# Kernel tuning notes

Hardware: AMD Instinct MI355X
Metric: run time of the kernel (lower is better)

## Reference

```python
import jax, jax.numpy as jnp
import numpy as np
import math

B, S, D = 1, 2048, 2048
H, HD, KV = 16, 128, 1
E, F, TOPK = 8, 4096, 2
EPS = 1e-5


def setup_inputs() -> dict:
    key = jax.random.key(0)
    ks = jax.random.split(key, 14)
    sc = 0.02
    inp = {
        "x": jax.random.normal(ks[0], (B, S, D), dtype=jnp.float32),
        "wq": jax.random.normal(ks[1], (D, H * HD), dtype=jnp.float32) * sc,
        "wk": jax.random.normal(ks[2], (D, KV * HD), dtype=jnp.float32) * sc,
        "wv": jax.random.normal(ks[3], (D, KV * HD), dtype=jnp.float32) * sc,
        "wo": jax.random.normal(ks[4], (H * HD, D), dtype=jnp.float32) * sc,
        "w_router": jax.random.normal(ks[5], (D, E), dtype=jnp.float32) * sc,
        "w1": jax.random.normal(ks[6], (E, D, F), dtype=jnp.float32) * sc,
        "w3": jax.random.normal(ks[7], (E, D, F), dtype=jnp.float32) * sc,
        "w2": jax.random.normal(ks[8], (E, F, D), dtype=jnp.float32) * sc,
        "s_pre_mqa": jnp.ones((D,), dtype=jnp.float32),
        "s_post_mqa": jnp.ones((D,), dtype=jnp.float32),
        "s_pre_moe": jnp.ones((D,), dtype=jnp.float32),
        "s_post_moe": jnp.ones((D,), dtype=jnp.float32),
    }
    return inp


def _rmsnorm(x, scale):
    ms = jnp.mean(x * x, axis=-1, keepdims=True)
    return x * jax.lax.rsqrt(ms + EPS) * scale


def _mqa(h, wq, wk, wv, wo):
    b, s, _ = h.shape
    q = (h @ wq).reshape(b, s, H, HD)
    k = (h @ wk).reshape(b, s, KV, HD)
    v = (h @ wv).reshape(b, s, KV, HD)
    # repeat_interleave kv heads up to H (MQA)
    k = jnp.repeat(k, H // KV, axis=2)
    v = jnp.repeat(v, H // KV, axis=2)
    scale = 1.0 / math.sqrt(HD)
    scores = jnp.einsum("bqhd,bkhd->bhqk", q, k) * scale  # [B,H,S,S]
    causal = jnp.tril(jnp.ones((s, s), dtype=bool))
    scores = jnp.where(causal, scores, jnp.float32(-jnp.inf))
    attn = jax.nn.softmax(scores, axis=-1)
    out = jnp.einsum("bhqk,bkhd->bqhd", attn, v).reshape(b, s, H * HD)
    return out @ wo


def _moe(h, w_router, w1, w2, w3):
    logits = h @ w_router                        # [B,S,E]
    probs = jax.nn.softmax(logits, axis=-1)
    topv, topi = jax.lax.top_k(probs, TOPK)      # [B,S,K]
    topv = topv / jnp.sum(topv, axis=-1, keepdims=True)
    # combine weights per expert: [B,S,E]
    combine = jnp.sum(jax.nn.one_hot(topi, E, dtype=h.dtype) * topv[..., None], axis=-2)
    out = jnp.zeros_like(h)
    for e in range(E):  # fixed small expert count
        ye = (jax.nn.silu(h @ w1[e]) * (h @ w3[e])) @ w2[e]
        out = out + combine[..., e:e + 1] * ye
    return out, combine


def reference(x, wq, wk, wv, wo, w_router, w1, w2, w3,
              s_pre_mqa, s_post_mqa, s_pre_moe, s_post_moe):
    mqa_out = _mqa(_rmsnorm(x, s_pre_mqa), wq, wk, wv, wo)
    x = x + _rmsnorm(mqa_out, s_post_mqa)  # dropout p=0 (eval)
    moe_out, router_mask = _moe(_rmsnorm(x, s_pre_moe), w_router, w1, w2, w3)
    x = x + _rmsnorm(moe_out, s_post_moe)
    return x, router_mask
```

## Files before the change

### kernel.cpp

```cpp
#include <hip/hip_runtime.h>

#define S_LEN 2048
#define DM 2048
#define NHEAD 16
#define HDIM 128
#define NEXP 8
#define FF 4096
#define EPSV 1e-5f

typedef unsigned short u16;
typedef short bf16x8 __attribute__((ext_vector_type(8)));
typedef float f32x4 __attribute__((ext_vector_type(4)));

__device__ __forceinline__ f32x4 mfma16(bf16x8 a, bf16x8 b, f32x4 c) {
  return __builtin_amdgcn_mfma_f32_16x16x32_bf16(a, b, c, 0, 0, 0);
}

__device__ __forceinline__ float bf2f(u16 u) {
  union { unsigned int i; float f; } v; v.i = ((unsigned int)u) << 16; return v.f;
}
__device__ __forceinline__ u16 f2bf(float f) {
  union { float f; unsigned int i; } v; v.f = f;
  unsigned int u = v.i;
  return (u16)((u + 0x7fffu + ((u >> 16) & 1u)) >> 16);
}

__device__ __forceinline__ void gload_lds16(const u16* g, u16* l) {
  __builtin_amdgcn_global_load_lds(
      (const __attribute__((address_space(1))) unsigned int*)(unsigned long long)g,
      (__attribute__((address_space(3))) unsigned int*)(unsigned long long)l, 16, 0, 0);
}

__device__ __forceinline__ float blocksum(float v, float* sh) {
#pragma unroll
  for (int off = 32; off; off >>= 1) v += __shfl_xor(v, off, 64);
  const int w = threadIdx.x >> 6;
  if ((threadIdx.x & 63) == 0) sh[w] = v;
  __syncthreads();
  v = sh[0] + sh[1] + sh[2] + sh[3];
  __syncthreads();
  return v;
}

__global__ __launch_bounds__(256) void convsplit_kernel(
    const float* __restrict__ src, int ld, u16* __restrict__ dhi, u16* __restrict__ dlo) {
  __shared__ float tile[64][65];
  const int n0 = blockIdx.x * 64, k0 = blockIdx.y * 64;
  const int t = threadIdx.x;
  {
    int r = t >> 4, c4 = (t & 15) * 4;
#pragma unroll
    for (int i = 0; i < 4; ++i) {
      float4 v = *reinterpret_cast<const float4*>(src + (size_t)(k0 + r + i * 16) * ld + n0 + c4);
      tile[r + i * 16][c4 + 0] = v.x;
      tile[r + i * 16][c4 + 1] = v.y;
      tile[r + i * 16][c4 + 2] = v.z;
      tile[r + i * 16][c4 + 3] = v.w;
    }
  }
  __syncthreads();
#pragma unroll
  for (int i = 0; i < 2; ++i) {
    int idx = i * 256 + t;
    int n = idx >> 3, kc = (idx & 7) * 8;
    bf16x8 hi, lo;
#pragma unroll
    for (int j = 0; j < 8; ++j) {
      float f = tile[kc + j][n];
      u16 hv = f2bf(f);
      hi[j] = (short)hv;
      lo[j] = (short)f2bf(f - bf2f(hv));
    }
    size_t o = (size_t)(n0 + n) * 2048 + k0 + kc;
    *reinterpret_cast<bf16x8*>(dhi + o) = hi;
    *reinterpret_cast<bf16x8*>(dlo + o) = lo;
  }
}

__device__ __forceinline__ void convT_body(char* lds, const float* __restrict__ src,
                                           int R, int C, u16* __restrict__ dst,
                                           int nblk, int rblk, int e) {
  float(*tile)[65] = reinterpret_cast<float(*)[65]>(lds);
  const int n0 = nblk * 64, r0 = rblk * 64;
  const size_t bofs = (size_t)e * R * C;
  const int t = threadIdx.x;
  {
    int r = t >> 4, c4 = (t & 15) * 4;
#pragma unroll
    for (int i = 0; i < 4; ++i) {
      float4 v = *reinterpret_cast<const float4*>(src + bofs + (size_t)(r0 + r + i * 16) * C + n0 + c4);
      tile[r + i * 16][c4 + 0] = v.x;
      tile[r + i * 16][c4 + 1] = v.y;
      tile[r + i * 16][c4 + 2] = v.z;
      tile[r + i * 16][c4 + 3] = v.w;
    }
  }
  __syncthreads();
#pragma unroll
  for (int i = 0; i < 2; ++i) {
    int idx = i * 256 + t;
    int n = idx >> 3, kc = (idx & 7) * 8;
    bf16x8 pk;
#pragma unroll
    for (int j = 0; j < 8; ++j) pk[j] = (short)f2bf(tile[kc + j][n]);
    *reinterpret_cast<bf16x8*>(dst + bofs + (size_t)(n0 + n) * R + r0 + kc) = pk;
  }
}

__global__ __launch_bounds__(256) void rms_pre_kernel(
    const float* __restrict__ x, const float* __restrict__ s, u16* __restrict__ h1) {
  __shared__ float sh[4];
  const int row = blockIdx.x, t = threadIdx.x;
  const float* xr = x + (size_t)row * DM + t * 8;
  float4 a = *reinterpret_cast<const float4*>(xr);
  float4 b = *reinterpret_cast<const float4*>(xr + 4);
  float v[8] = {a.x, a.y, a.z, a.w, b.x, b.y, b.z, b.w};
  float ss = 0.f;
#pragma unroll
  for (int j = 0; j < 8; ++j) ss += v[j] * v[j];
  float inv = rsqrtf(blocksum(ss, sh) * (1.f / DM) + EPSV);
  const float* sp = s + t * 8;
  bf16x8 hi, lo;
#pragma unroll
  for (int j = 0; j < 8; ++j) {
    float val = v[j] * inv * sp[j];
    u16 hv = f2bf(val);
    hi[j] = (short)hv;
    lo[j] = (short)f2bf(val - bf2f(hv));
  }
  *reinterpret_cast<bf16x8*>(h1 + (size_t)row * 4096 + t * 8) = hi;
  *reinterpret_cast<bf16x8*>(h1 + (size_t)row * 4096 + 2048 + t * 8) = lo;
}

__device__ __forceinline__ void gemm_sp_body(
    char* lds, const u16* __restrict__ A, const u16* __restrict__ Bthi,
    const u16* __restrict__ Btlo, float* __restrict__ Cpart, int N,
    int mblk, int nblk, int z) {
  const int m0 = mblk * 128, n0 = nblk * 128;
  const int t = threadIdx.x, lane = t & 63, w = t >> 6;
  const int wm = (w >> 1) * 64, wn = (w & 1) * 64;
  const int l15 = lane & 15, lg = lane >> 4;
  const int wbase = t & ~63;

  u16* As = (u16*)lds;
  u16* Bs = (u16*)(lds + 16384);

  const u16* Ab = A + (size_t)m0 * 4096 + (z == 1 ? 2048 : 0);
  const u16* Bb = (z == 2 ? Btlo : Bthi) + (size_t)n0 * 2048;

  f32x4 acc[4][4];
#pragma unroll
  for (int m = 0; m < 4; ++m)
#pragma unroll
    for (int n = 0; n < 4; ++n) acc[m][n] = (f32x4){0.f, 0.f, 0.f, 0.f};

  for (int k0 = 0; k0 < 2048; k0 += 64) {
    __syncthreads();
#pragma unroll
    for (int i = 0; i < 4; ++i) {
      int p = i * 256 + t;
      int row = p >> 3;
      int csrc = (p & 7) ^ (row & 7);
      gload_lds16(Ab + (size_t)row * 4096 + k0 + csrc * 8, As + (i * 256 + wbase) * 8);
      gload_lds16(Bb + (size_t)row * 2048 + k0 + csrc * 8, Bs + (i * 256 + wbase) * 8);
    }
    __syncthreads();
    bf16x8 af[2][4], bfr[2][4];
#pragma unroll
    for (int kk = 0; kk < 2; ++kk) {
#pragma unroll
      for (int m = 0; m < 4; ++m) {
        int row = wm + m * 16 + l15;
        int byte = row * 128 + (((kk * 4 + lg) * 16) ^ ((row & 7) << 4));
        af[kk][m] = *reinterpret_cast<const bf16x8*>((const char*)As + byte);
      }
#pragma unroll
      for (int n = 0; n < 4; ++n) {
        int row = wn + n * 16 + l15;
        int byte = row * 128 + (((kk * 4 + lg) * 16) ^ ((row & 7) << 4));
        bfr[kk][n] = *reinterpret_cast<const bf16x8*>((const char*)Bs + byte);
      }
    }
#pragma unroll
    for (int kk = 0; kk < 2; ++kk)
#pragma unroll
      for (int m = 0; m < 4; ++m)
#pragma unroll
        for (int n = 0; n < 4; ++n) acc[m][n] = mfma16(af[kk][m], bfr[kk][n], acc[m][n]);
  }

  float* C = Cpart + (size_t)z * 2048 * N;
#pragma unroll
  for (int m = 0; m < 4; ++m)
#pragma unroll
    for (int n = 0; n < 4; ++n)
#pragma unroll
      for (int r = 0; r < 4; ++r) {
        int row = m0 + wm + m * 16 + lg * 4 + r;
        int col = n0 + wn + n * 16 + l15;
        C[(size_t)row * N + col] = acc[m][n][r];
      }
}

__global__ __launch_bounds__(256) void gemm_sp(
    const u16* __restrict__ A, const u16* __restrict__ Bthi, const u16* __restrict__ Btlo,
    float* __restrict__ Cpart, int N) {
  __shared__ alignas(16) char lds[32768];
  gemm_sp_body(lds, A, Bthi, Btlo, Cpart, N, blockIdx.x, blockIdx.y, blockIdx.z);
}

__global__ __launch_bounds__(256) void fat_qkv_conv(
    const u16* __restrict__ A, const u16* __restrict__ Bthi, const u16* __restrict__ Btlo,
    float* __restrict__ Cpart, const float* __restrict__ w1, const float* __restrict__ w3,
    u16* __restrict__ w1t, u16* __restrict__ w3t) {
  __shared__ alignas(16) char lds[32768];
  int bid = blockIdx.x;
  if (bid < 864) {
    gemm_sp_body(lds, A, Bthi, Btlo, Cpart, 2304, bid % 16, (bid / 16) % 18, bid / 288);
  } else {
    int cid = bid - 864;
    if (cid < 16384)
      convT_body(lds, w1, 2048, 4096, w1t, cid % 64, (cid / 64) % 32, cid / 2048);
    else {
      cid -= 16384;
      convT_body(lds, w3, 2048, 4096, w3t, cid % 64, (cid / 64) % 32, cid / 2048);
    }
  }
}

__global__ __launch_bounds__(256) void combine_qkv(const float* __restrict__ Cp,
                                                   u16* __restrict__ QKV) {
  const int r = blockIdx.x;
  const int c = blockIdx.y * 256 + threadIdx.x;
  const size_t P = (size_t)2048 * 2304;
  size_t o = (size_t)r * 2304 + c;
  float v = Cp[o] + Cp[P + o] + Cp[2 * P + o];
  u16 hv = f2bf(v);
  QKV[(size_t)r * 4608 + c] = hv;
  QKV[(size_t)r * 4608 + 2304 + c] = f2bf(v - bf2f(hv));
}

__global__ __launch_bounds__(256) void vtrans_kernel(const u16* __restrict__ QKV,
                                                     u16* __restrict__ vt) {
  __shared__ u16 tile[64][65];
  const int s0 = blockIdx.x * 64, c0 = blockIdx.y * 64;
  const int t = threadIdx.x;
#pragma unroll
  for (int i = 0; i < 16; ++i) {
    int idx = i * 256 + t;
    int r = idx >> 6, c = idx & 63;
    int col = c0 + c;
    int src = (col < 128) ? (2176 + col) : (4480 + col - 128);
    tile[r][c] = QKV[(size_t)(s0 + r) * 4608 + src];
  }
  __syncthreads();
#pragma unroll
  for (int i = 0; i < 16; ++i) {
    int idx = i * 256 + t;
    int cc = idx >> 6, ss = idx & 63;
    vt[(size_t)(c0 + cc) * S_LEN + s0 + ss] = tile[ss][cc];
  }
}

__device__ __forceinline__ void attn_body(char* lds, const u16* __restrict__ QKV,
                                          const u16* __restrict__ vt, u16* __restrict__ Os,
                                          int bx, int h) {
  const int qb = 31 - bx;
  const int t = threadIdx.x, w = t >> 6, lane = t & 63;
  const int l15 = lane & 15, lg = lane >> 4;
  const int qr0 = qb * 64 + w * 16;
  const int qrow = qr0 + l15;

  u16* Ks = (u16*)lds;
  u16* Vs = (u16*)(lds + 34816);
  u16* myP = (u16*)(lds + 71680) + w * (16 * 72);

  bf16x8 qf[2][4];
#pragma unroll
  for (int p = 0; p < 2; ++p)
#pragma unroll
    for (int c = 0; c < 4; ++c)
      qf[p][c] = *reinterpret_cast<const bf16x8*>(QKV + (size_t)qrow * 4608 + p * 2304 +
                                                  h * 128 + c * 32 + lg * 8);

  f32x4 o[8];
#pragma unroll
  for (int n = 0; n < 8; ++n) o[n] = (f32x4){0.f, 0.f, 0.f, 0.f};
  f32x4 lracc = (f32x4){0.f, 0.f, 0.f, 0.f};
  bf16x8 onesf;
#pragma unroll
  for (int j = 0; j < 8; ++j) onesf[j] = (short)0x3F80;

  const float scale = 0.08838834764831845f;
  const int kend = qb * 64 + 64;

  for (int j0 = 0; j0 < kend; j0 += 64) {
    __syncthreads();
#pragma unroll
    for (int i = 0; i < 8; ++i) {
      int idx = i * 256 + t;
      int row = idx >> 5, seg = idx & 31;
      int srccol = (seg < 16) ? (2048 + seg * 8) : (4352 + (seg - 16) * 8);
      bf16x8 v = *reinterpret_cast<const bf16x8*>(QKV + (size_t)(j0 + row) * 4608 + srccol);
      *reinterpret_cast<bf16x8*>(&Ks[row * 272 + seg * 8]) = v;
    }
#pragma unroll
    for (int i = 0; i < 8; ++i) {
      int idx = i * 256 + t;
      int row = idx >> 3, seg = idx & 7;
      bf16x8 v = *reinterpret_cast<const bf16x8*>(vt + (size_t)row * S_LEN + j0 + seg * 8);
      *reinterpret_cast<bf16x8*>(&Vs[row * 72 + seg * 8]) = v;
    }
    __syncthreads();

#pragma unroll
    for (int jj = 0; jj < 64; jj += 32) {
      if (j0 + jj > qr0 + 15) continue;
      f32x4 sc[2];
#pragma unroll
      for (int half = 0; half < 2; ++half) {
        const int kb = (jj + half * 16 + l15) * 272;
        f32x4 a0 = (f32x4){0.f, 0.f, 0.f, 0.f};
        f32x4 a1 = (f32x4){0.f, 0.f, 0.f, 0.f};
        f32x4 a2 = (f32x4){0.f, 0.f, 0.f, 0.f};
#pragma unroll
        for (int cc = 0; cc < 4; ++cc) {
          bf16x8 kh = *reinterpret_cast<const bf16x8*>(&Ks[kb + cc * 32 + lg * 8]);
          a0 = mfma16(qf[0][cc], kh, a0);
          a1 = mfma16(qf[1][cc], kh, a1);
        }
#pragma unroll
        for (int cc = 0; cc < 4; ++cc) {
          bf16x8 kl = *reinterpret_cast<const bf16x8*>(&Ks[kb + 128 + cc * 32 + lg * 8]);
          a2 = mfma16(qf[0][cc], kl, a2);
        }
        f32x4 a = (a0 + a1) + a2;
#pragma unroll
        for (int r = 0; r < 4; ++r) {
          int rowg = qr0 + lg * 4 + r;
          int colg = j0 + jj + half * 16 + l15;
          sc[half][r] = (colg <= rowg) ? a[r] * scale : -1e30f;
        }
      }
#pragma unroll
      for (int r = 0; r < 4; ++r) {
        float p0 = __expf(sc[0][r]);
        float p1 = __expf(sc[1][r]);
        int lrow = lg * 4 + r;
        u16 h0 = f2bf(p0), h1v = f2bf(p1);
        myP[lrow * 72 + l15] = h0;
        myP[lrow * 72 + 16 + l15] = h1v;
        myP[lrow * 72 + 32 + l15] = f2bf(p0 - bf2f(h0));
        myP[lrow * 72 + 48 + l15] = f2bf(p1 - bf2f(h1v));
      }
      bf16x8 pfh = *reinterpret_cast<const bf16x8*>(myP + l15 * 72 + lg * 8);
      bf16x8 pfl = *reinterpret_cast<const bf16x8*>(myP + l15 * 72 + 32 + lg * 8);

      lracc = mfma16(pfh, onesf, lracc);
      lracc = mfma16(pfl, onesf, lracc);

#pragma unroll
      for (int n = 0; n < 8; ++n) {
        bf16x8 vh = *reinterpret_cast<const bf16x8*>(&Vs[(n * 16 + l15) * 72 + jj + lg * 8]);
        bf16x8 vl = *reinterpret_cast<const bf16x8*>(&Vs[(n * 16 + l15 + 128) * 72 + jj + lg * 8]);
        o[n] = mfma16(pfh, vh, o[n]);
        o[n] = mfma16(pfl, vh, o[n]);
        o[n] = mfma16(pfh, vl, o[n]);
      }
    }
  }
#pragma unroll
  for (int n = 0; n < 8; ++n)
#pragma unroll
    for (int r = 0; r < 4; ++r) {
      int rowg = qr0 + lg * 4 + r;
      float v = o[n][r] / lracc[r];
      u16 hv = f2bf(v);
      Os[(size_t)rowg * 4096 + h * 128 + n * 16 + l15] = hv;
      Os[(size_t)rowg * 4096 + 2048 + h * 128 + n * 16 + l15] = f2bf(v - bf2f(hv));
    }
}

__global__ __launch_bounds__(256) void fat_attn_conv(
    const u16* __restrict__ QKV, const u16* __restrict__ vt, u16* __restrict__ Os,
    const float* __restrict__ w2, u16* __restrict__ w2t) {
  __shared__ alignas(16) char lds[80896];
  int bid = blockIdx.x;
  if (bid < 512) {
    attn_body(lds, QKV, vt, Os, bid & 31, bid >> 5);
  } else {
    int cid = bid - 512;
    convT_body(lds, w2, 4096, 2048, w2t, cid % 32, (cid / 32) % 64, cid / 2048);
  }
}

__global__ __launch_bounds__(256) void rms_mid_kernel(
    const float* __restrict__ x, const float* __restrict__ Cp,
    const float* __restrict__ spost, const float* __restrict__ spre,
    float* __restrict__ x1, u16* __restrict__ h2b, float* __restrict__ inv2out) {
  __shared__ float sh1[4];
  __shared__ float sh2[4];
  const int row = blockIdx.x, t = threadIdx.x;
  const size_t base = (size_t)row * DM + t * 8;
  const size_t P = (size_t)2048 * 2048;
  float mv[8];
  {
    float4 a0 = *reinterpret_cast<const float4*>(Cp + base);
    float4 b0 = *reinterpret_cast<const float4*>(Cp + base + 4);
    float4 a1 = *reinterpret_cast<const float4*>(Cp + P + base);
    float4 b1 = *reinterpret_cast<const float4*>(Cp + P + base + 4);
    float4 a2 = *reinterpret_cast<const float4*>(Cp + 2 * P + base);
    float4 b2 = *reinterpret_cast<const float4*>(Cp + 2 * P + base + 4);
    mv[0] = a0.x + a1.x + a2.x; mv[1] = a0.y + a1.y + a2.y;
    mv[2] = a0.z + a1.z + a2.z; mv[3] = a0.w + a1.w + a2.w;
    mv[4] = b0.x + b1.x + b2.x; mv[5] = b0.y + b1.y + b2.y;
    mv[6] = b0.z + b1.z + b2.z; mv[7] = b0.w + b1.w + b2.w;
  }
  float ss1 = 0.f;
#pragma unroll
  for (int j = 0; j < 8; ++j) ss1 += mv[j] * mv[j];
  float inv1 = rsqrtf(blocksum(ss1, sh1) * (1.f / DM) + EPSV);
  float4 xa = *reinterpret_cast<const float4*>(x + base);
  float4 xb = *reinterpret_cast<const float4*>(x + base + 4);
  float xv[8] = {xa.x, xa.y, xa.z, xa.w, xb.x, xb.y, xb.z, xb.w};
  float x1v[8];
  float ss2 = 0.f;
#pragma unroll
  for (int j = 0; j < 8; ++j) {
    x1v[j] = xv[j] + mv[j] * inv1 * spost[t * 8 + j];
    ss2 += x1v[j] * x1v[j];
  }
  float inv2 = rsqrtf(blocksum(ss2, sh2) * (1.f / DM) + EPSV);
  *reinterpret_cast<float4*>(x1 + base) = make_float4(x1v[0], x1v[1], x1v[2], x1v[3]);
  *reinterpret_cast<float4*>(x1 + base + 4) = make_float4(x1v[4], x1v[5], x1v[6], x1v[7]);
  bf16x8 hb;
#pragma unroll
  for (int j = 0; j < 8; ++j) hb[j] = (short)f2bf(x1v[j] * inv2 * spre[t * 8 + j]);
  *reinterpret_cast<bf16x8*>(h2b + base) = hb;
  if (t == 0) inv2out[row] = inv2;
}

__global__ void zero_meta_kernel(int* __restrict__ cnt) {
  if (threadIdx.x < NEXP) cnt[threadIdx.x] = 0;
}

__global__ __launch_bounds__(256) void router_kernel(
    const float* __restrict__ x1, const float* __restrict__ inv2,
    const float* __restrict__ spre, const float* __restrict__ wr,
    float* __restrict__ comb, int* __restrict__ topi, float* __restrict__ topw,
    int* __restrict__ cnt) {
  const int token = blockIdx.x, t = threadIdx.x;
  const float* xr = x1 + (size_t)token * DM + t * 8;
  const float iv = inv2[token];
  float4 a = *reinterpret_cast<const float4*>(xr);
  float4 b = *reinterpret_cast<const float4*>(xr + 4);
  float xv[8] = {a.x, a.y, a.z, a.w, b.x, b.y, b.z, b.w};
  float hv[8];
#pragma unroll
  for (int j = 0; j < 8; ++j) hv[j] = xv[j] * iv * spre[t * 8 + j];
  float acc[8] = {0.f, 0.f, 0.f, 0.f, 0.f, 0.f, 0.f, 0.f};
  const float* wrow = wr + (size_t)t * 8 * 8;
#pragma unroll
  for (int j = 0; j < 8; ++j) {
    const float* wj = wrow + j * 8;
#pragma unroll
    for (int e = 0; e < 8; ++e) acc[e] += hv[j] * wj[e];
  }
#pragma unroll
  for (int off = 32; off; off >>= 1)
#pragma unroll
    for (int e = 0; e < 8; ++e) acc[e] += __shfl_xor(acc[e], off, 64);
  __shared__ float red[4][8];
  __shared__ float lgits[8];
  const int w = t >> 6;
  if ((t & 63) == 0) {
#pragma unroll
    for (int e = 0; e < 8; ++e) red[w][e] = acc[e];
  }
  __syncthreads();
  if (t < 8) lgits[t] = red[0][t] + red[1][t] + red[2][t] + red[3][t];
  __syncthreads();
  if (t == 0) {
    float L[8], mx = -1e30f;
#pragma unroll
    for (int e = 0; e < 8; ++e) {
      L[e] = lgits[e];
      mx = fmaxf(mx, L[e]);
    }
    float p[8], s = 0.f;
#pragma unroll
    for (int e = 0; e < 8; ++e) {
      p[e] = expf(L[e] - mx);
      s += p[e];
    }
#pragma unroll
    for (int e = 0; e < 8; ++e) p[e] /= s;
    int e0 = 0;
    for (int e = 1; e < 8; ++e)
      if (p[e] > p[e0]) e0 = e;
    int e1 = (e0 == 0) ? 1 : 0;
    for (int e = 0; e < 8; ++e)
      if (e != e0 && p[e] > p[e1]) e1 = e;
    float ssum = p[e0] + p[e1];
    float w0 = p[e0] / ssum, w1 = p[e1] / ssum;
    for (int e = 0; e < 8; ++e)
      comb[(size_t)token * 8 + e] = (e == e0) ? w0 : ((e == e1) ? w1 : 0.f);
    topi[2 * token] = e0;
    topi[2 * token + 1] = e1;
    topw[2 * token] = w0;
    topw[2 * token + 1] = w1;
    atomicAdd(&cnt[e0], 1);
    atomicAdd(&cnt[e1], 1);
  }
}

__global__ void build_meta_kernel(const int* __restrict__ cnt, int* __restrict__ cursor,
                                  int* __restrict__ meta) {
  if (threadIdx.x != 0) return;
  int off = 0, nt = 0;
  for (int e = 0; e < NEXP; ++e) {
    int c = cnt[e];
    cursor[e] = off;
    int ntl = (c + 255) >> 8;
    for (int r = 0; r < ntl; ++r) {
      meta[8 + nt] = e;
      meta[64 + nt] = off + r * 256;
      int rem = c - r * 256;
      meta[120 + nt] = rem < 256 ? rem : 256;
      ++nt;
    }
    off += c;
  }
  meta[0] = nt;
}

__global__ void scatter_kernel(const int* __restrict__ topi, int* __restrict__ cursor,
                               int* __restrict__ ptok, int* __restrict__ pos_of) {
  int token = blockIdx.x * 256 + threadIdx.x;
  if (token >= S_LEN) return;
  for (int k = 0; k < 2; ++k) {
    int e = topi[2 * token + k];
    int pos = atomicAdd(&cursor[e], 1);
    ptok[pos] = token;
    pos_of[2 * token + k] = pos;
  }
}

__global__ __launch_bounds__(512) void moe_gemm1b(
    const u16* __restrict__ H2, const u16* __restrict__ W1t, const u16* __restrict__ W3t,
    u16* __restrict__ U, const int* __restrict__ meta, const int* __restrict__ ptok) {
  const int tile = blockIdx.x;
  if (tile >= meta[0]) return;
  const int e = meta[8 + tile], row0 = meta[64 + tile], rows = meta[120 + tile];
  const int n0 = blockIdx.y * 64;
  const u16* B1 = W1t + (size_t)e * FF * DM + (size_t)n0 * 2048;
  const u16* B3 = W3t + (size_t)e * FF * DM + (size_t)n0 * 2048;
  const int t = threadIdx.x, lane = t & 63, w = t >> 6;
  const int wm = (w >> 1) * 64, wn = (w & 1) * 32;
  const int l15 = lane & 15, lg = lane >> 4;
  const int wbase = t & ~63;

  __shared__ alignas(16) u16 As[16384];
  __shared__ alignas(16) u16 B1s[4096];
  __shared__ alignas(16) u16 B3s[4096];
  __shared__ int toks[256];
  if (t < 256) toks[t] = (t < rows) ? ptok[row0 + t] : ptok[row0];
  __syncthreads();

  f32x4 aG[4][2], aT[4][2];
#pragma unroll
  for (int m = 0; m < 4; ++m)
#pragma unroll
    for (int n = 0; n < 2; ++n) {
      aG[m][n] = (f32x4){0.f, 0.f, 0.f, 0.f};
      aT[m][n] = (f32x4){0.f, 0.f, 0.f, 0.f};
    }

  for (int k0 = 0; k0 < DM; k0 += 64) {
    __syncthreads();
#pragma unroll
    for (int i = 0; i < 4; ++i) {
      int p = i * 512 + t;
      int row = p >> 3;
      int csrc = (p & 7) ^ (row & 7);
      gload_lds16(H2 + (size_t)toks[row] * DM + k0 + csrc * 8, As + (i * 512 + wbase) * 8);
    }
    {
      int row = t >> 3;
      int csrc = (t & 7) ^ (row & 7);
      gload_lds16(B1 + (size_t)row * 2048 + k0 + csrc * 8, B1s + wbase * 8);
      gload_lds16(B3 + (size_t)row * 2048 + k0 + csrc * 8, B3s + wbase * 8);
    }
    __syncthreads();
#pragma unroll
    for (int kk = 0; kk < 2; ++kk) {
      bf16x8 af[4], b1f[2], b3f[2];
#pragma unroll
      for (int m = 0; m < 4; ++m) {
        int row = wm + m * 16 + l15;
        int byte = row * 128 + (((kk * 4 + lg) * 16) ^ ((row & 7) << 4));
        af[m] = *reinterpret_cast<const bf16x8*>((const char*)As + byte);
      }
#pragma unroll
      for (int n = 0; n < 2; ++n) {
        int row = wn + n * 16 + l15;
        int byte = row * 128 + (((kk * 4 + lg) * 16) ^ ((row & 7) << 4));
        b1f[n] = *reinterpret_cast<const bf16x8*>((const char*)B1s + byte);
        b3f[n] = *reinterpret_cast<const bf16x8*>((const char*)B3s + byte);
      }
#pragma unroll
      for (int m = 0; m < 4; ++m)
#pragma unroll
        for (int n = 0; n < 2; ++n) {
          aG[m][n] = mfma16(af[m], b1f[n], aG[m][n]);
          aT[m][n] = mfma16(af[m], b3f[n], aT[m][n]);
        }
    }
  }
#pragma unroll
  for (int m = 0; m < 4; ++m)
#pragma unroll
    for (int n = 0; n < 2; ++n)
#pragma unroll
      for (int r = 0; r < 4; ++r) {
        int lrow = wm + m * 16 + lg * 4 + r;
        if (lrow < rows) {
          float g = aG[m][n][r], tt = aT[m][n][r];
          float u = (g / (1.f + __expf(-g))) * tt;
          U[(size_t)(row0 + lrow) * FF + n0 + wn + n * 16 + l15] = f2bf(u);
        }
      }
}

__global__ __launch_bounds__(512) void moe_gemm2b(
    const u16* __restrict__ U, const u16* __restrict__ W2t, u16* __restrict__ Y,
    const int* __restrict__ meta) {
  const int tile = blockIdx.x;
  if (tile >= meta[0]) return;
  const int e = meta[8 + tile], row0 = meta[64 + tile], rows = meta[120 + tile];
  const int n0 = blockIdx.y * 128;
  const u16* Bb = W2t + (size_t)e * DM * FF + (size_t)n0 * 4096;
  const int t = threadIdx.x, lane = t & 63, w = t >> 6;
  const int wm = (w >> 1) * 64, wn = (w & 1) * 64;
  const int l15 = lane & 15, lg = lane >> 4;
  const int wbase = t & ~63;

  __shared__ alignas(16) u16 As[16384];
  __shared__ alignas(16) u16 Bs[8192];

  f32x4 acc[4][4];
#pragma unroll
  for (int m = 0; m < 4; ++m)
#pragma unroll
    for (int n = 0; n < 4; ++n) acc[m][n] = (f32x4){0.f, 0.f, 0.f, 0.f};

  for (int k0 = 0; k0 < FF; k0 += 64) {
    __syncthreads();
#pragma unroll
    for (int i = 0; i < 4; ++i) {
      int p = i * 512 + t;
      int row = p >> 3;
      int csrc = (p & 7) ^ (row & 7);
      gload_lds16(U + (size_t)(row0 + row) * FF + k0 + csrc * 8, As + (i * 512 + wbase) * 8);
    }
#pragma unroll
    for (int i = 0; i < 2; ++i) {
      int p = i * 512 + t;
      int row = p >> 3;
      int csrc = (p & 7) ^ (row & 7);
      gload_lds16(Bb + (size_t)row * 4096 + k0 + csrc * 8, Bs + (i * 512 + wbase) * 8);
    }
    __syncthreads();
#pragma unroll
    for (int kk = 0; kk < 2; ++kk) {
      bf16x8 af[4], bfr[4];
#pragma unroll
      for (int m = 0; m < 4; ++m) {
        int row = wm + m * 16 + l15;
        int byte = row * 128 + (((kk * 4 + lg) * 16) ^ ((row & 7) << 4));
        af[m] = *reinterpret_cast<const bf16x8*>((const char*)As + byte);
      }
#pragma unroll
      for (int n = 0; n < 4; ++n) {
        int row = wn + n * 16 + l15;
        int byte = row * 128 + (((kk * 4 + lg) * 16) ^ ((row & 7) << 4));
        bfr[n] = *reinterpret_cast<const bf16x8*>((const char*)Bs + byte);
      }
#pragma unroll
      for (int m = 0; m < 4; ++m)
#pragma unroll
        for (int n = 0; n < 4; ++n) acc[m][n] = mfma16(af[m], bfr[n], acc[m][n]);
    }
  }
#pragma unroll
  for (int m = 0; m < 4; ++m)
#pragma unroll
    for (int n = 0; n < 4; ++n)
#pragma unroll
      for (int r = 0; r < 4; ++r) {
        int lrow = wm + m * 16 + lg * 4 + r;
        if (lrow < rows)
          Y[(size_t)(row0 + lrow) * DM + n0 + wn + n * 16 + l15] = f2bf(acc[m][n][r]);
      }
}

__global__ __launch_bounds__(256) void moe_final_kernel(
    const float* __restrict__ x1, const u16* __restrict__ Y,
    const int* __restrict__ pos_of, const float* __restrict__ topw,
    const float* __restrict__ spost, float* __restrict__ xout) {
  __shared__ float sh[4];
  const int row = blockIdx.x, t = threadIdx.x;
  const int p0 = pos_of[2 * row], p1 = pos_of[2 * row + 1];
  const float w0 = topw[2 * row], w1 = topw[2 * row + 1];
  bf16x8 y0 = *reinterpret_cast<const bf16x8*>(Y + (size_t)p0 * DM + t * 8);
  bf16x8 y1 = *reinterpret_cast<const bf16x8*>(Y + (size_t)p1 * DM + t * 8);
  float mv[8];
  float ss = 0.f;
#pragma unroll
  for (int j = 0; j < 8; ++j) {
    mv[j] = w0 * bf2f((u16)y0[j]) + w1 * bf2f((u16)y1[j]);
    ss += mv[j] * mv[j];
  }
  float inv = rsqrtf(blocksum(ss, sh) * (1.f / DM) + EPSV);
  const size_t base = (size_t)row * DM + t * 8;
#pragma unroll
  for (int j = 0; j < 8; ++j)
    xout[base + j] = x1[base + j] + mv[j] * inv * spost[t * 8 + j];
}

extern "C" void kernel_launch(void* const* d_in, const int* in_sizes, int n_in,
                              void* d_out, int out_size, void* d_ws, size_t ws_size,
                              hipStream_t stream) {
  (void)in_sizes; (void)n_in; (void)out_size; (void)ws_size;
  const float* x = (const float*)d_in[0];
  const float* wq = (const float*)d_in[1];
  const float* wk = (const float*)d_in[2];
  const float* wv = (const float*)d_in[3];
  const float* wo = (const float*)d_in[4];
  const float* wrt = (const float*)d_in[5];
  const float* w1 = (const float*)d_in[6];
  const float* w3 = (const float*)d_in[7];
  const float* w2 = (const float*)d_in[8];
  const float* s_pre_mqa = (const float*)d_in[9];
  const float* s_post_mqa = (const float*)d_in[10];
  const float* s_pre_moe = (const float*)d_in[11];
  const float* s_post_moe = (const float*)d_in[12];

  float* xout = (float*)d_out;
  float* out_router = xout + (size_t)S_LEN * DM;

  char* wsp = (char*)d_ws;
  size_t off = 0;
  auto alloc = [&](size_t n) {
    char* p = wsp + off;
    off += (n + 255) & ~(size_t)255;
    return p;
  };
  float* Cpart = (float*)alloc((size_t)3 * 2048 * 2304 * 4);
  u16* U = (u16*)Cpart;
  u16* Y = U + (size_t)4096 * 4096;
  u16* h1s = (u16*)alloc((size_t)S_LEN * 4096 * 2);
  u16* attn_s = h1s;
  u16* Btq_hi = (u16*)alloc((size_t)2304 * 2048 * 2);
  u16* Btq_lo = (u16*)alloc((size_t)2304 * 2048 * 2);
  u16* Bto_hi = (u16*)alloc((size_t)2048 * 2048 * 2);
  u16* Bto_lo = (u16*)alloc((size_t)2048 * 2048 * 2);
  u16* QKV = (u16*)alloc((size_t)S_LEN * 4608 * 2);
  u16* vt = (u16*)alloc((size_t)256 * S_LEN * 2);
  float* x1 = (float*)alloc((size_t)S_LEN * DM * 4);
  u16* h2b = (u16*)alloc((size_t)S_LEN * DM * 2);
  float* inv2 = (float*)alloc(S_LEN * 4);
  int* topi = (int*)alloc(4096 * 4);
  float* topw = (float*)alloc(4096 * 4);
  int* pos_of = (int*)alloc(4096 * 4);
  int* ptok = (int*)alloc(4352 * 4);
  int* cnt = (int*)alloc(32 * 4);
  int* cursor = (int*)alloc(32 * 4);
  int* meta = (int*)alloc(256 * 4);
  u16* w1t = (u16*)alloc((size_t)NEXP * DM * FF * 2);
  u16* w3t = (u16*)alloc((size_t)NEXP * DM * FF * 2);
  u16* w2t = (u16*)alloc((size_t)NEXP * FF * DM * 2);

  dim3 B256(256);
  dim3 B512(512);

  convsplit_kernel<<<dim3(32, 32), B256, 0, stream>>>(wq, 2048, Btq_hi, Btq_lo);
  convsplit_kernel<<<dim3(2, 32), B256, 0, stream>>>(wk, 128, Btq_hi + (size_t)2048 * 2048,
                                                     Btq_lo + (size_t)2048 * 2048);
  convsplit_kernel<<<dim3(2, 32), B256, 0, stream>>>(wv, 128, Btq_hi + (size_t)2176 * 2048,
                                                     Btq_lo + (size_t)2176 * 2048);
  convsplit_kernel<<<dim3(32, 32), B256, 0, stream>>>(wo, 2048, Bto_hi, Bto_lo);

  rms_pre_kernel<<<dim3(S_LEN), B256, 0, stream>>>(x, s_pre_mqa, h1s);
  fat_qkv_conv<<<dim3(864 + 32768), B256, 0, stream>>>(h1s, Btq_hi, Btq_lo, Cpart,
                                                       w1, w3, w1t, w3t);
  combine_qkv<<<dim3(2048, 9), B256, 0, stream>>>(Cpart, QKV);
  vtrans_kernel<<<dim3(32, 4), B256, 0, stream>>>(QKV, vt);
  fat_attn_conv<<<dim3(512 + 16384), B256, 0, stream>>>(QKV, vt, attn_s, w2, w2t);
  gemm_sp<<<dim3(16, 16, 3), B256, 0, stream>>>(attn_s, Bto_hi, Bto_lo, Cpart, 2048);
  rms_mid_kernel<<<dim3(S_LEN), B256, 0, stream>>>(x, Cpart, s_post_mqa, s_pre_moe, x1, h2b, inv2);
  zero_meta_kernel<<<dim3(1), dim3(64), 0, stream>>>(cnt);
  router_kernel<<<dim3(S_LEN), B256, 0, stream>>>(x1, inv2, s_pre_moe, wrt, out_router,
                                                  topi, topw, cnt);
  build_meta_kernel<<<dim3(1), dim3(64), 0, stream>>>(cnt, cursor, meta);
  scatter_kernel<<<dim3(8), B256, 0, stream>>>(topi, cursor, ptok, pos_of);
  moe_gemm1b<<<dim3(24, 64), B512, 0, stream>>>(h2b, w1t, w3t, U, meta, ptok);
  moe_gemm2b<<<dim3(24, 16), B512, 0, stream>>>(U, w2t, Y, meta);
  moe_final_kernel<<<dim3(S_LEN), B256, 0, stream>>>(x1, Y, pos_of, topw, s_post_moe, xout);
}
```

Measured before the change: 965.2 us.

## Fuse split-bf16 triple GEMM into one kernel accumulating hi/lo products

Replaces the three separate z-sliced partial GEMMs (hi*hi, lo*hi, hi*lo) written to a float partial buffer with a single GEMM body that loads both hi and lo tiles of A and B and issues all three MFMAs into one accumulator. The QKV GEMM now writes its split bf16 output directly, which removes the combine_qkv kernel, and the output projection writes a single fp32 result that rms_mid reads without summing three partials. This removes partial-buffer round trips through HBM and one launch. The cost is a 128x64 tile with larger LDS (48KB), more A reloads per output, and a workspace layout change that gives U/Y/mqa separate allocations.

Result: faster. 885.0 us (-8.3%).

```diff
diff --git a/kernel.cpp b/kernel.cpp
--- a/kernel.cpp
+++ b/kernel.cpp
@@ -132,27 +132,31 @@
   *reinterpret_cast<bf16x8*>(h1 + (size_t)row * 4096 + 2048 + t * 8) = lo;
 }
 
-__device__ __forceinline__ void gemm_sp_body(
+__device__ __forceinline__ void gemm3_body(
     char* lds, const u16* __restrict__ A, const u16* __restrict__ Bthi,
-    const u16* __restrict__ Btlo, float* __restrict__ Cpart, int N,
-    int mblk, int nblk, int z) {
-  const int m0 = mblk * 128, n0 = nblk * 128;
+    const u16* __restrict__ Btlo, void* __restrict__ out,
+    int mblk, int nblk, int mode, int ldc, int lo_off) {
+  const int m0 = mblk * 128, n0 = nblk * 64;
   const int t = threadIdx.x, lane = t & 63, w = t >> 6;
-  const int wm = (w >> 1) * 64, wn = (w & 1) * 64;
+  const int wm = (w >> 1) * 64, wn = (w & 1) * 32;
   const int l15 = lane & 15, lg = lane >> 4;
   const int wbase = t & ~63;
 
-  u16* As = (u16*)lds;
-  u16* Bs = (u16*)(lds + 16384);
-
-  const u16* Ab = A + (size_t)m0 * 4096 + (z == 1 ? 2048 : 0);
-  const u16* Bb = (z == 2 ? Btlo : Bthi) + (size_t)n0 * 2048;
-
-  f32x4 acc[4][4];
+  u16* Ah = (u16*)lds;
+  u16* Al = (u16*)(lds + 16384);
+  u16* Bh = (u16*)(lds + 32768);
+  u16* Bl = (u16*)(lds + 40960);
+
+  const u16* Abh = A + (size_t)m0 * 4096;
+  const u16* Abl = Abh + 2048;
+  const u16* Bbh = Bthi + (size_t)n0 * 2048;
+  const u16* Bbl = Btlo + (size_t)n0 * 2048;
+
+  f32x4 acc[4][2];
 #pragma unroll
   for (int m = 0; m < 4; ++m)
 #pragma unroll
-    for (int n = 0; n < 4; ++n) acc[m][n] = (f32x4){0.f, 0.f, 0.f, 0.f};
+    for (int n = 0; n < 2; ++n) acc[m][n] = (f32x4){0.f, 0.f, 0.f, 0.f};
 
   for (int k0 = 0; k0 < 2048; k0 += 64) {
     __syncthreads();
@@ -161,64 +165,82 @@
       int p = i * 256 + t;
       int row = p >> 3;
       int csrc = (p & 7) ^ (row & 7);
-      gload_lds16(Ab + (size_t)row * 4096 + k0 + csrc * 8, As + (i * 256 + wbase) * 8);
-      gload_lds16(Bb + (size_t)row * 2048 + k0 + csrc * 8, Bs + (i * 256 + wbase) * 8);
+      gload_lds16(Abh + (size_t)row * 4096 + k0 + csrc * 8, Ah + (i * 256 + wbase) * 8);
+      gload_lds16(Abl + (size_t)row * 4096 + k0 + csrc * 8, Al + (i * 256 + wbase) * 8);
+    }
+#pragma unroll
+    for (int i = 0; i < 2; ++i) {
+      int p = i * 256 + t;
+      int row = p >> 3;
+      int csrc = (p & 7) ^ (row & 7);
+      gload_lds16(Bbh + (size_t)row * 2048 + k0 + csrc * 8, Bh + (i * 256 + wbase) * 8);
+      gload_lds16(Bbl + (size_t)row * 2048 + k0 + csrc * 8, Bl + (i * 256 + wbase) * 8);
     }
     __syncthreads();
-    bf16x8 af[2][4], bfr[2][4];
 #pragma unroll
     for (int kk = 0; kk < 2; ++kk) {
+      bf16x8 ah[4], al[4], bh[2], bl[2];
 #pragma unroll
       for (int m = 0; m < 4; ++m) {
         int row = wm + m * 16 + l15;
         int byte = row * 128 + (((kk * 4 + lg) * 16) ^ ((row & 7) << 4));
-        af[kk][m] = *reinterpret_cast<const bf16x8*>((const char*)As + byte);
-      }
-#pragma unroll
-      for (int n = 0; n < 4; ++n) {
+        ah[m] = *reinterpret_cast<const bf16x8*>((const char*)Ah + byte);
+        al[m] = *reinterpret_cast<const bf16x8*>((const char*)Al + byte);
+      }
+#pragma unroll
+      for (int n = 0; n < 2; ++n) {
         int row = wn + n * 16 + l15;
         int byte = row * 128 + (((kk * 4 + lg) * 16) ^ ((row & 7) << 4));
-        bfr[kk][n] = *reinterpret_cast<const bf16x8*>((const char*)Bs + byte);
-      }
-    }
-#pragma unroll
-    for (int kk = 0; kk < 2; ++kk)
+        bh[n] = *reinterpret_cast<const bf16x8*>((const char*)Bh + byte);
+        bl[n] = *reinterpret_cast<const bf16x8*>((const char*)Bl + byte);
+      }
 #pragma unroll
       for (int m = 0; m < 4; ++m)
 #pragma unroll
-        for (int n = 0; n < 4; ++n) acc[m][n] = mfma16(af[kk][m], bfr[kk][n], acc[m][n]);
-  }
-
-  float* C = Cpart + (size_t)z * 2048 * N;
+        for (int n = 0; n < 2; ++n) {
+          acc[m][n] = mfma16(ah[m], bh[n], acc[m][n]);
+          acc[m][n] = mfma16(al[m], bh[n], acc[m][n]);
+          acc[m][n] = mfma16(ah[m], bl[n], acc[m][n]);
+        }
+    }
+  }
 #pragma unroll
   for (int m = 0; m < 4; ++m)
 #pragma unroll
-    for (int n = 0; n < 4; ++n)
+    for (int n = 0; n < 2; ++n)
 #pragma unroll
       for (int r = 0; r < 4; ++r) {
         int row = m0 + wm + m * 16 + lg * 4 + r;
         int col = n0 + wn + n * 16 + l15;
-        C[(size_t)row * N + col] = acc[m][n][r];
-      }
-}
-
-__global__ __launch_bounds__(256) void gemm_sp(
+        float v = acc[m][n][r];
+        if (mode == 1) {
+          u16* C = (u16*)out;
+          u16 hv = f2bf(v);
+          C[(size_t)row * ldc + col] = hv;
+          C[(size_t)row * ldc + lo_off + col] = f2bf(v - bf2f(hv));
+        } else {
+          ((float*)out)[(size_t)row * ldc + col] = v;
+        }
+      }
+}
+
+__global__ __launch_bounds__(256) void gemm3_kernel(
     const u16* __restrict__ A, const u16* __restrict__ Bthi, const u16* __restrict__ Btlo,
-    float* __restrict__ Cpart, int N) {
-  __shared__ alignas(16) char lds[32768];
-  gemm_sp_body(lds, A, Bthi, Btlo, Cpart, N, blockIdx.x, blockIdx.y, blockIdx.z);
+    float* __restrict__ out) {
+  __shared__ alignas(16) char lds[49152];
+  gemm3_body(lds, A, Bthi, Btlo, out, blockIdx.x, blockIdx.y, 2, 2048, 0);
 }
 
 __global__ __launch_bounds__(256) void fat_qkv_conv(
     const u16* __restrict__ A, const u16* __restrict__ Bthi, const u16* __restrict__ Btlo,
-    float* __restrict__ Cpart, const float* __restrict__ w1, const float* __restrict__ w3,
+    u16* __restrict__ QKV, const float* __restrict__ w1, const float* __restrict__ w3,
     u16* __restrict__ w1t, u16* __restrict__ w3t) {
-  __shared__ alignas(16) char lds[32768];
+  __shared__ alignas(16) char lds[49152];
   int bid = blockIdx.x;
-  if (bid < 864) {
-    gemm_sp_body(lds, A, Bthi, Btlo, Cpart, 2304, bid % 16, (bid / 16) % 18, bid / 288);
+  if (bid < 576) {
+    gemm3_body(lds, A, Bthi, Btlo, QKV, bid % 16, bid / 16, 1, 4608, 2304);
   } else {
-    int cid = bid - 864;
+    int cid = bid - 576;
     if (cid < 16384)
       convT_body(lds, w1, 2048, 4096, w1t, cid % 64, (cid / 64) % 32, cid / 2048);
     else {
@@ -226,18 +248,6 @@
       convT_body(lds, w3, 2048, 4096, w3t, cid % 64, (cid / 64) % 32, cid / 2048);
     }
   }
-}
-
-__global__ __launch_bounds__(256) void combine_qkv(const float* __restrict__ Cp,
-                                                   u16* __restrict__ QKV) {
-  const int r = blockIdx.x;
-  const int c = blockIdx.y * 256 + threadIdx.x;
-  const size_t P = (size_t)2048 * 2304;
-  size_t o = (size_t)r * 2304 + c;
-  float v = Cp[o] + Cp[P + o] + Cp[2 * P + o];
-  u16 hv = f2bf(v);
-  QKV[(size_t)r * 4608 + c] = hv;
-  QKV[(size_t)r * 4608 + 2304 + c] = f2bf(v - bf2f(hv));
 }
 
 __global__ __launch_bounds__(256) void vtrans_kernel(const u16* __restrict__ QKV,
@@ -395,26 +405,19 @@
 }
 
 __global__ __launch_bounds__(256) void rms_mid_kernel(
-    const float* __restrict__ x, const float* __restrict__ Cp,
+    const float* __restrict__ x, const float* __restrict__ mqa,
     const float* __restrict__ spost, const float* __restrict__ spre,
     float* __restrict__ x1, u16* __restrict__ h2b, float* __restrict__ inv2out) {
   __shared__ float sh1[4];
   __shared__ float sh2[4];
   const int row = blockIdx.x, t = threadIdx.x;
   const size_t base = (size_t)row * DM + t * 8;
-  const size_t P = (size_t)2048 * 2048;
   float mv[8];
   {
-    float4 a0 = *reinterpret_cast<const float4*>(Cp + base);
-    float4 b0 = *reinterpret_cast<const float4*>(Cp + base + 4);
-    float4 a1 = *reinterpret_cast<const float4*>(Cp + P + base);
-    float4 b1 = *reinterpret_cast<const float4*>(Cp + P + base + 4);
-    float4 a2 = *reinterpret_cast<const float4*>(Cp + 2 * P + base);
-    float4 b2 = *reinterpret_cast<const float4*>(Cp + 2 * P + base + 4);
-    mv[0] = a0.x + a1.x + a2.x; mv[1] = a0.y + a1.y + a2.y;
-    mv[2] = a0.z + a1.z + a2.z; mv[3] = a0.w + a1.w + a2.w;
-    mv[4] = b0.x + b1.x + b2.x; mv[5] = b0.y + b1.y + b2.y;
-    mv[6] = b0.z + b1.z + b2.z; mv[7] = b0.w + b1.w + b2.w;
+    float4 a0 = *reinterpret_cast<const float4*>(mqa + base);
+    float4 b0 = *reinterpret_cast<const float4*>(mqa + base + 4);
+    mv[0] = a0.x; mv[1] = a0.y; mv[2] = a0.z; mv[3] = a0.w;
+    mv[4] = b0.x; mv[5] = b0.y; mv[6] = b0.z; mv[7] = b0.w;
   }
   float ss1 = 0.f;
 #pragma unroll
@@ -756,9 +759,9 @@
     off += (n + 255) & ~(size_t)255;
     return p;
   };
-  float* Cpart = (float*)alloc((size_t)3 * 2048 * 2304 * 4);
-  u16* U = (u16*)Cpart;
-  u16* Y = U + (size_t)4096 * 4096;
+  u16* U = (u16*)alloc((size_t)4096 * FF * 2);
+  u16* Y = (u16*)alloc((size_t)4096 * DM * 2);
+  float* mqa = (float*)alloc((size_t)S_LEN * DM * 4);
   u16* h1s = (u16*)alloc((size_t)S_LEN * 4096 * 2);
   u16* attn_s = h1s;
   u16* Btq_hi = (u16*)alloc((size_t)2304 * 2048 * 2);
@@ -792,13 +795,12 @@
   convsplit_kernel<<<dim3(32, 32), B256, 0, stream>>>(wo, 2048, Bto_hi, Bto_lo);
 
   rms_pre_kernel<<<dim3(S_LEN), B256, 0, stream>>>(x, s_pre_mqa, h1s);
-  fat_qkv_conv<<<dim3(864 + 32768), B256, 0, stream>>>(h1s, Btq_hi, Btq_lo, Cpart,
+  fat_qkv_conv<<<dim3(576 + 32768), B256, 0, stream>>>(h1s, Btq_hi, Btq_lo, QKV,
                                                        w1, w3, w1t, w3t);
-  combine_qkv<<<dim3(2048, 9), B256, 0, stream>>>(Cpart, QKV);
   vtrans_kernel<<<dim3(32, 4), B256, 0, stream>>>(QKV, vt);
   fat_attn_conv<<<dim3(512 + 16384), B256, 0, stream>>>(QKV, vt, attn_s, w2, w2t);
-  gemm_sp<<<dim3(16, 16, 3), B256, 0, stream>>>(attn_s, Bto_hi, Bto_lo, Cpart, 2048);
-  rms_mid_kernel<<<dim3(S_LEN), B256, 0, stream>>>(x, Cpart, s_post_mqa, s_pre_moe, x1, h2b, inv2);
+  gemm3_kernel<<<dim3(16, 32), B256, 0, stream>>>(attn_s, Bto_hi, Bto_lo, mqa);
+  rms_mid_kernel<<<dim3(S_LEN), B256, 0, stream>>>(x, mqa, s_post_mqa, s_pre_moe, x1, h2b, inv2);
   zero_meta_kernel<<<dim3(1), dim3(64), 0, stream>>>(cnt);
   router_kernel<<<dim3(S_LEN), B256, 0, stream>>>(x1, inv2, s_pre_moe, wrt, out_router,
                                                   topi, topw, cnt);
```
